# Performance work log

Measured on AMD Instinct MI355X. Metric: run time of the kernel, lower is better.

The kernel has to match this reference:

```python
import jax, jax.numpy as jnp
import numpy as np

WEIGHT = 1.0

# 3x3x3 discrete Laplacian stencil (6-connected, center -6), as in the torch module
_LAP_K = jnp.array(
    [[[0, 0, 0], [0, 1, 0], [0, 0, 0]],
     [[0, 1, 0], [1, -6, 1], [0, 1, 0]],
     [[0, 0, 0], [0, 1, 0], [0, 0, 0]]], dtype=jnp.float32)


def _abs_laplacian3d(x):
    """x: (N, D, H, W) -> |3D Laplacian(x)| with zero padding, same shape."""
    y = jax.lax.conv_general_dilated(
        x[:, None],              # (N, 1, D, H, W)
        _LAP_K[None, None],      # (1, 1, 3, 3, 3)
        window_strides=(1, 1, 1),
        padding=[(1, 1), (1, 1), (1, 1)])
    return jnp.abs(y[:, 0])


def setup_inputs() -> dict:
    key = jax.random.key(0)
    k1, k2 = jax.random.split(key)
    B, C, D, H, W = 2, 4, 64, 256, 256
    logits = jax.random.normal(k1, (B, C, D, H, W), dtype=jnp.float32)
    targets = jax.random.randint(k2, (B, D, H, W), 0, C)
    return {"logits": logits, "targets": targets}


def reference(logits, targets):
    B, C, D, H, W = logits.shape
    # softmax over class dim, drop background class 0 -> (B, C-1, D, H, W)
    probs = jax.nn.softmax(logits, axis=1)[:, 1:]
    # one-hot target masks for classes 1..C-1 -> (B, C-1, D, H, W)
    cls = jnp.arange(1, C)[None, :, None, None, None]
    tmask = (targets[:, None] == cls).astype(logits.dtype)
    # fused 3D Laplacian + abs over all (batch, class) pairs at once
    pred_b = _abs_laplacian3d(probs.reshape(B * (C - 1), D, H, W))
    targ_b = _abs_laplacian3d(tmask.reshape(B * (C - 1), D, H, W))
    # sum over classes of per-class MSE, divided by (C-1) == mean over everything
    return WEIGHT * jnp.mean((pred_b - targ_b) ** 2)
```

## Files before the change

### kernel.cpp

```cpp
#include <hip/hip_runtime.h>


#define CS   (1 << 22)
#define NTOT_INV (1.0f / 25165824.0f)
#define BIAS3 ((8 << 20) | (8 << 10) | 8)
#define BAR() asm volatile("s_waitcnt lgkmcnt(0)\n\ts_barrier" ::: "memory")

#define ISSUE(S, off)                                                        \
    S##0 = *(const float4*)(L + lBase + (off));                              \
    S##1 = *(const float4*)(L + lBase + (off) + CS);                         \
    S##2 = *(const float4*)(L + lBase + (off) + 2 * CS);                     \
    S##3 = *(const float4*)(L + lBase + (off) + 3 * CS);                     \
    S##t = *(const int4*)(T + tBase + (off));                                \
    if (hd) {                                                                \
        S##h0 = L[hlB + (off)];          S##h1 = L[hlB + (off) + CS];        \
        S##h2 = L[hlB + (off) + 2 * CS]; S##h3 = L[hlB + (off) + 3 * CS];    \
        S##hq = T[htB + (off)];                                              \
    }

__device__ __forceinline__ void smax1(float x0, float x1, float x2, float x3,
                                      float vm, float& p1, float& p2, float& p3) {
    float m  = fmaxf(fmaxf(x0, x1), fmaxf(x2, x3));
    float e0 = __expf(x0 - m);
    float e1 = __expf(x1 - m);
    float e2 = __expf(x2 - m);
    float e3 = __expf(x3 - m);
    float r  = vm * __builtin_amdgcn_rcpf(e0 + e1 + e2 + e3);
    p1 = e1 * r; p2 = e2 * r; p3 = e3 * r;
}

__device__ __forceinline__ int ohenc(int t, int msk) {
    int nz = (t > 0) ? 1 : 0;
    return (nz << (((t - 1) & 3) * 10)) & msk;
}

__global__ __launch_bounds__(256) void boundary_loss_kernel(
        const float* __restrict__ L,
        const int*   __restrict__ T,
        float*       __restrict__ out) {
    const int tid = threadIdx.x;
    const int tw  = tid & 7;
    const int th  = tid >> 3;

    const int bi    = blockIdx.x;
    const int wt    = bi & 7;
    const int dt    = (bi >> 3) & 15;
    const int colHi = bi >> 7;
    const int ht    = colHi % 9;
    const int b     = colHi / 9;

    const int   h0 = ht * 30;
    const int   h  = h0 + th - 1;
    const bool  hv = ((unsigned)h < 256u);
    const float vm = hv ? 1.f : 0.f;
    const int   ohm = hv ? ~0 : 0;
    const int   w0 = wt << 5;
    const int   sp = ((hv ? h : 0) << 8) | (w0 + (tw << 2));
    const int   tBase = b * CS + sp;
    const int   lBase = (b << 2) * CS + sp;
    const bool  live  = (th >= 1) && (th <= 30) && hv;
    const int   d0 = dt << 2;

    const bool  hd   = (tid < 60);
    const int   side = (tid >= 30) ? 1 : 0;
    const int   hr   = side ? (tid - 29) : (tid + 1);
    const int   hh   = h0 + hr - 1;
    const int   hwv  = side ? (w0 + 32) : (w0 - 1);
    const bool  hvv  = hd && ((unsigned)hh < 256u) && ((unsigned)hwv < 256u);
    const float hvm  = hvv ? 1.f : 0.f;
    const int   hohm = hvv ? ~0 : 0;
    const int   hsp  = ((hvv ? hh : 0) << 8) | (hvv ? hwv : 0);
    const int   htB  = b * CS + hsp;
    const int   hlB  = (b << 2) * CS + hsp;

    __shared__ float P1[32][32], P2[32][32], P3[32][32];
    __shared__ int   OHS[32][32];
    __shared__ float HL1[2][32], HL2[2][32], HL3[2][32];
    __shared__ int   HLO[2][32];

    const int c0 = tw << 2;
    const float* lp1 = (tw == 0) ? &HL1[0][th] : &P1[th][c0 - 1];
    const float* lp2 = (tw == 0) ? &HL2[0][th] : &P2[th][c0 - 1];
    const float* lp3 = (tw == 0) ? &HL3[0][th] : &P3[th][c0 - 1];
    const int*   lpo = (tw == 0) ? &HLO[0][th] : &OHS[th][c0 - 1];
    const float* rp1 = (tw == 7) ? &HL1[1][th] : &P1[th][c0 + 4];
    const float* rp2 = (tw == 7) ? &HL2[1][th] : &P2[th][c0 + 4];
    const float* rp3 = (tw == 7) ? &HL3[1][th] : &P3[th][c0 + 4];
    const int*   rpo = (tw == 7) ? &HLO[1][th] : &OHS[th][c0 + 4];

    float4 c1, c2, c3; int4 coh;
    float4 a1, a2, a3; int4 aoh;
    float hc1 = 0.f, hc2 = 0.f, hc3 = 0.f; int hco = 0;
    float accv = 0.f;

    {
        const int  off = (dt > 0 ? d0 - 1 : 0) << 16;
        const float svm  = (dt > 0) ? vm : 0.f;
        const int   sohm = (dt > 0) ? ohm : 0;
        float4 q0 = *(const float4*)(L + lBase + off);
        float4 q1 = *(const float4*)(L + lBase + off + CS);
        float4 q2 = *(const float4*)(L + lBase + off + 2 * CS);
        float4 q3 = *(const float4*)(L + lBase + off + 3 * CS);
        int4   qt = *(const int4*)(T + tBase + off);
        smax1(q0.x, q1.x, q2.x, q3.x, svm, a1.x, a2.x, a3.x);
        smax1(q0.y, q1.y, q2.y, q3.y, svm, a1.y, a2.y, a3.y);
        smax1(q0.z, q1.z, q2.z, q3.z, svm, a1.z, a2.z, a3.z);
        smax1(q0.w, q1.w, q2.w, q3.w, svm, a1.w, a2.w, a3.w);
        aoh.x = ohenc(qt.x, sohm) + BIAS3; aoh.y = ohenc(qt.y, sohm) + BIAS3;
        aoh.z = ohenc(qt.z, sohm) + BIAS3; aoh.w = ohenc(qt.w, sohm) + BIAS3;
    }

    {
        const int off = d0 << 16;
        float4 q0 = *(const float4*)(L + lBase + off);
        float4 q1 = *(const float4*)(L + lBase + off + CS);
        float4 q2 = *(const float4*)(L + lBase + off + 2 * CS);
        float4 q3 = *(const float4*)(L + lBase + off + 3 * CS);
        int4   qt = *(const int4*)(T + tBase + off);
        float hx0 = 0.f, hx1 = 0.f, hx2 = 0.f, hx3 = 0.f; int hqt = 0;
        if (hd) {
            hx0 = L[hlB + off]; hx1 = L[hlB + off + CS];
            hx2 = L[hlB + off + 2 * CS]; hx3 = L[hlB + off + 3 * CS];
            hqt = T[htB + off];
        }
        smax1(q0.x, q1.x, q2.x, q3.x, vm, c1.x, c2.x, c3.x);
        smax1(q0.y, q1.y, q2.y, q3.y, vm, c1.y, c2.y, c3.y);
        smax1(q0.z, q1.z, q2.z, q3.z, vm, c1.z, c2.z, c3.z);
        smax1(q0.w, q1.w, q2.w, q3.w, vm, c1.w, c2.w, c3.w);
        coh.x = ohenc(qt.x, ohm); coh.y = ohenc(qt.y, ohm);
        coh.z = ohenc(qt.z, ohm); coh.w = ohenc(qt.w, ohm);
        smax1(hx0, hx1, hx2, hx3, hvm, hc1, hc2, hc3);
        hco = ohenc(hqt, hohm);
    }

    float4 A0, A1, A2, A3; int4 At;
    float Ah0 = 0.f, Ah1 = 0.f, Ah2 = 0.f, Ah3 = 0.f; int Ahq = 0;
    {
        const int off = (d0 + 1 < 64 ? d0 + 1 : 63) << 16;
        ISSUE(A, off)
    }

#pragma unroll
    for (int i = 0; i < 4; ++i) {
        float4 B0, B1, B2, B3; int4 Bt;
        float Bh0 = 0.f, Bh1 = 0.f, Bh2 = 0.f, Bh3 = 0.f; int Bhq = 0;
        B0 = B1 = B2 = B3 = make_float4(0.f, 0.f, 0.f, 0.f);
        Bt = make_int4(0, 0, 0, 0);
        if (i < 3) {
            const int off = (d0 + i + 2 < 64 ? d0 + i + 2 : 63) << 16;
            ISSUE(B, off)
        }

        BAR();
        *(float4*)&P1[th][c0] = c1;
        *(float4*)&P2[th][c0] = c2;
        *(float4*)&P3[th][c0] = c3;
        *(int4*)&OHS[th][c0]  = coh;
        if (hd) {
            HL1[side][hr] = hc1; HL2[side][hr] = hc2; HL3[side][hr] = hc3;
            HLO[side][hr] = hco;
        }
        BAR();

        if (live) {
            float4 u, dn4; float lf, rt;
            u = *(float4*)&P1[th - 1][c0]; dn4 = *(float4*)&P1[th + 1][c0];
            lf = *lp1; rt = *rp1;
            a1.x += u.x + dn4.x + lf   + c1.y - 6.f * c1.x;
            a1.y += u.y + dn4.y + c1.x + c1.z - 6.f * c1.y;
            a1.z += u.z + dn4.z + c1.y + c1.w - 6.f * c1.z;
            a1.w += u.w + dn4.w + c1.z + rt   - 6.f * c1.w;
            u = *(float4*)&P2[th - 1][c0]; dn4 = *(float4*)&P2[th + 1][c0];
            lf = *lp2; rt = *rp2;
            a2.x += u.x + dn4.x + lf   + c2.y - 6.f * c2.x;
            a2.y += u.y + dn4.y + c2.x + c2.z - 6.f * c2.y;
            a2.z += u.z + dn4.z + c2.y + c2.w - 6.f * c2.z;
            a2.w += u.w + dn4.w + c2.z + rt   - 6.f * c2.w;
            u = *(float4*)&P3[th - 1][c0]; dn4 = *(float4*)&P3[th + 1][c0];
            lf = *lp3; rt = *rp3;
            a3.x += u.x + dn4.x + lf   + c3.y - 6.f * c3.x;
            a3.y += u.y + dn4.y + c3.x + c3.z - 6.f * c3.y;
            a3.z += u.z + dn4.z + c3.y + c3.w - 6.f * c3.z;
            a3.w += u.w + dn4.w + c3.z + rt   - 6.f * c3.w;

            int4 iu = *(int4*)&OHS[th - 1][c0];
            int4 id = *(int4*)&OHS[th + 1][c0];
            int  il = *lpo, ir = *rpo;
            aoh.x += iu.x + id.x + il    + coh.y - 6 * coh.x;
            aoh.y += iu.y + id.y + coh.x + coh.z - 6 * coh.y;
            aoh.z += iu.z + id.z + coh.y + coh.w - 6 * coh.z;
            aoh.w += iu.w + id.w + coh.z + ir    - 6 * coh.w;
        }

        const int   dnA   = d0 + i + 1;
        const float vmn   = (dnA < 64) ? vm : 0.f;
        const int   ohmn  = (dnA < 64) ? ohm : 0;
        const float hvmn  = (dnA < 64) ? hvm : 0.f;
        const int   hohmn = (dnA < 64) ? hohm : 0;
        float4 n1, n2, n3; int4 noh;
        smax1(A0.x, A1.x, A2.x, A3.x, vmn, n1.x, n2.x, n3.x);
        smax1(A0.y, A1.y, A2.y, A3.y, vmn, n1.y, n2.y, n3.y);
        smax1(A0.z, A1.z, A2.z, A3.z, vmn, n1.z, n2.z, n3.z);
        smax1(A0.w, A1.w, A2.w, A3.w, vmn, n1.w, n2.w, n3.w);
        noh.x = ohenc(At.x, ohmn); noh.y = ohenc(At.y, ohmn);
        noh.z = ohenc(At.z, ohmn); noh.w = ohenc(At.w, ohmn);
        float hn1, hn2, hn3;
        smax1(Ah0, Ah1, Ah2, Ah3, hvmn, hn1, hn2, hn3);
        int hno = ohenc(Ahq, hohmn);

        if (live) {
            int t0 = aoh.x + noh.x, t1 = aoh.y + noh.y;
            int t2 = aoh.z + noh.z, t3 = aoh.w + noh.w;
            float lp, lt, df;
            lp = fabsf(a1.x + n1.x); lt = fabsf((float)((t0 & 1023) - 8));          df = lp - lt; accv = fmaf(df, df, accv);
            lp = fabsf(a2.x + n2.x); lt = fabsf((float)(((t0 >> 10) & 1023) - 8));  df = lp - lt; accv = fmaf(df, df, accv);
            lp = fabsf(a3.x + n3.x); lt = fabsf((float)(((t0 >> 20) & 1023) - 8));  df = lp - lt; accv = fmaf(df, df, accv);
            lp = fabsf(a1.y + n1.y); lt = fabsf((float)((t1 & 1023) - 8));          df = lp - lt; accv = fmaf(df, df, accv);
            lp = fabsf(a2.y + n2.y); lt = fabsf((float)(((t1 >> 10) & 1023) - 8));  df = lp - lt; accv = fmaf(df, df, accv);
            lp = fabsf(a3.y + n3.y); lt = fabsf((float)(((t1 >> 20) & 1023) - 8));  df = lp - lt; accv = fmaf(df, df, accv);
            lp = fabsf(a1.z + n1.z); lt = fabsf((float)((t2 & 1023) - 8));          df = lp - lt; accv = fmaf(df, df, accv);
            lp = fabsf(a2.z + n2.z); lt = fabsf((float)(((t2 >> 10) & 1023) - 8));  df = lp - lt; accv = fmaf(df, df, accv);
            lp = fabsf(a3.z + n3.z); lt = fabsf((float)(((t2 >> 20) & 1023) - 8));  df = lp - lt; accv = fmaf(df, df, accv);
            lp = fabsf(a1.w + n1.w); lt = fabsf((float)((t3 & 1023) - 8));          df = lp - lt; accv = fmaf(df, df, accv);
            lp = fabsf(a2.w + n2.w); lt = fabsf((float)(((t3 >> 10) & 1023) - 8));  df = lp - lt; accv = fmaf(df, df, accv);
            lp = fabsf(a3.w + n3.w); lt = fabsf((float)(((t3 >> 20) & 1023) - 8));  df = lp - lt; accv = fmaf(df, df, accv);
        }

        a1 = c1; a2 = c2; a3 = c3;
        aoh.x = coh.x + BIAS3; aoh.y = coh.y + BIAS3;
        aoh.z = coh.z + BIAS3; aoh.w = coh.w + BIAS3;
        c1 = n1; c2 = n2; c3 = n3; coh = noh;
        hc1 = hn1; hc2 = hn2; hc3 = hn3; hco = hno;
        A0 = B0; A1 = B1; A2 = B2; A3 = B3; At = Bt;
        Ah0 = Bh0; Ah1 = Bh1; Ah2 = Bh2; Ah3 = Bh3; Ahq = Bhq;
    }

    for (int o = 32; o > 0; o >>= 1) accv += __shfl_down(accv, o, 64);
    __shared__ float wsum[4];
    if ((tid & 63) == 0) wsum[tid >> 6] = accv;
    __syncthreads();
    if (tid == 0)
        atomicAdd(out, (wsum[0] + wsum[1] + wsum[2] + wsum[3]) * NTOT_INV);
}

extern "C" void kernel_launch(void* const* d_in, const int* in_sizes, int n_in,
                              void* d_out, int out_size, void* d_ws, size_t ws_size,
                              hipStream_t stream) {
    const float* logits  = (const float*)d_in[0];
    const int*   targets = (const int*)d_in[1];
    float*       out     = (float*)d_out;

    hipMemsetAsync(out, 0, sizeof(float), stream);
    boundary_loss_kernel<<<2304, 256, 0, stream>>>(logits, targets, out);
}
```

Measured before the change: 235.6 us.

## Retile stencil to full-width rows with wavefront shuffles for W neighbors

Result: faster. 217.1 us (-7.9%).

```diff
diff --git a/kernel.cpp b/kernel.cpp
--- a/kernel.cpp
+++ b/kernel.cpp
@@ -11,12 +11,7 @@
     S##1 = *(const float4*)(L + lBase + (off) + CS);                         \
     S##2 = *(const float4*)(L + lBase + (off) + 2 * CS);                     \
     S##3 = *(const float4*)(L + lBase + (off) + 3 * CS);                     \
-    S##t = *(const int4*)(T + tBase + (off));                                \
-    if (hd) {                                                                \
-        S##h0 = L[hlB + (off)];          S##h1 = L[hlB + (off) + CS];        \
-        S##h2 = L[hlB + (off) + 2 * CS]; S##h3 = L[hlB + (off) + 3 * CS];    \
-        S##hq = T[htB + (off)];                                              \
-    }
+    S##t = *(const int4*)(T + tBase + (off));
 
 __device__ __forceinline__ void smax1(float x0, float x1, float x2, float x3,
                                       float vm, float& p1, float& p2, float& p3) {
@@ -34,74 +29,45 @@
     return (nz << (((t - 1) & 3) * 10)) & msk;
 }
 
-__global__ __launch_bounds__(256) void boundary_loss_kernel(
+__global__ __launch_bounds__(512) void boundary_loss_kernel(
         const float* __restrict__ L,
         const int*   __restrict__ T,
         float*       __restrict__ out) {
-    const int tid = threadIdx.x;
-    const int tw  = tid & 7;
-    const int th  = tid >> 3;
-
-    const int bi    = blockIdx.x;
-    const int wt    = bi & 7;
-    const int dt    = (bi >> 3) & 15;
-    const int colHi = bi >> 7;
-    const int ht    = colHi % 9;
-    const int b     = colHi / 9;
-
-    const int   h0 = ht * 30;
-    const int   h  = h0 + th - 1;
-    const bool  hv = ((unsigned)h < 256u);
-    const float vm = hv ? 1.f : 0.f;
+    const int tid  = threadIdx.x;
+    const int lane = tid & 63;
+    const int th   = tid >> 6;
+    int bi = blockIdx.x;
+    const int dseg = bi & 7;  bi >>= 3;
+    const int ht   = bi % 43;
+    const int b    = bi / 43;
+
+    const int   h   = ht * 6 + th - 1;
+    const bool  hv  = ((unsigned)h < 256u);
+    const int   hcl = min(max(h, 0), 255);
+    const float vm  = hv ? 1.f : 0.f;
     const int   ohm = hv ? ~0 : 0;
-    const int   w0 = wt << 5;
-    const int   sp = ((hv ? h : 0) << 8) | (w0 + (tw << 2));
-    const int   tBase = b * CS + sp;
-    const int   lBase = (b << 2) * CS + sp;
-    const bool  live  = (th >= 1) && (th <= 30) && hv;
-    const int   d0 = dt << 2;
-
-    const bool  hd   = (tid < 60);
-    const int   side = (tid >= 30) ? 1 : 0;
-    const int   hr   = side ? (tid - 29) : (tid + 1);
-    const int   hh   = h0 + hr - 1;
-    const int   hwv  = side ? (w0 + 32) : (w0 - 1);
-    const bool  hvv  = hd && ((unsigned)hh < 256u) && ((unsigned)hwv < 256u);
-    const float hvm  = hvv ? 1.f : 0.f;
-    const int   hohm = hvv ? ~0 : 0;
-    const int   hsp  = ((hvv ? hh : 0) << 8) | (hvv ? hwv : 0);
-    const int   htB  = b * CS + hsp;
-    const int   hlB  = (b << 2) * CS + hsp;
-
-    __shared__ float P1[32][32], P2[32][32], P3[32][32];
-    __shared__ int   OHS[32][32];
-    __shared__ float HL1[2][32], HL2[2][32], HL3[2][32];
-    __shared__ int   HLO[2][32];
-
-    const int c0 = tw << 2;
-    const float* lp1 = (tw == 0) ? &HL1[0][th] : &P1[th][c0 - 1];
-    const float* lp2 = (tw == 0) ? &HL2[0][th] : &P2[th][c0 - 1];
-    const float* lp3 = (tw == 0) ? &HL3[0][th] : &P3[th][c0 - 1];
-    const int*   lpo = (tw == 0) ? &HLO[0][th] : &OHS[th][c0 - 1];
-    const float* rp1 = (tw == 7) ? &HL1[1][th] : &P1[th][c0 + 4];
-    const float* rp2 = (tw == 7) ? &HL2[1][th] : &P2[th][c0 + 4];
-    const float* rp3 = (tw == 7) ? &HL3[1][th] : &P3[th][c0 + 4];
-    const int*   rpo = (tw == 7) ? &HLO[1][th] : &OHS[th][c0 + 4];
+    const bool  live = (th >= 1) && (th <= 6) && hv;
+    const int   d0  = dseg << 3;
+
+    const int rowoff = (hcl << 8) + (lane << 2);
+    const int tBase  = b * CS + rowoff;
+    const int lBase  = (b << 2) * CS + rowoff;
+
+    __shared__ float P1[8][256], P2[8][256], P3[8][256];
+    __shared__ int   OH[8][256];
+
+    const int c0 = lane << 2;
 
     float4 c1, c2, c3; int4 coh;
     float4 a1, a2, a3; int4 aoh;
-    float hc1 = 0.f, hc2 = 0.f, hc3 = 0.f; int hco = 0;
     float accv = 0.f;
 
     {
-        const int  off = (dt > 0 ? d0 - 1 : 0) << 16;
-        const float svm  = (dt > 0) ? vm : 0.f;
-        const int   sohm = (dt > 0) ? ohm : 0;
-        float4 q0 = *(const float4*)(L + lBase + off);
-        float4 q1 = *(const float4*)(L + lBase + off + CS);
-        float4 q2 = *(const float4*)(L + lBase + off + 2 * CS);
-        float4 q3 = *(const float4*)(L + lBase + off + 3 * CS);
-        int4   qt = *(const int4*)(T + tBase + off);
+        const int   off  = (dseg > 0 ? d0 - 1 : 0) << 16;
+        const float svm  = (dseg > 0) ? vm : 0.f;
+        const int   sohm = (dseg > 0) ? ohm : 0;
+        float4 q0, q1, q2, q3; int4 qt;
+        ISSUE(q, off)
         smax1(q0.x, q1.x, q2.x, q3.x, svm, a1.x, a2.x, a3.x);
         smax1(q0.y, q1.y, q2.y, q3.y, svm, a1.y, a2.y, a3.y);
         smax1(q0.z, q1.z, q2.z, q3.z, svm, a1.z, a2.z, a3.z);
@@ -112,41 +78,28 @@
 
     {
         const int off = d0 << 16;
-        float4 q0 = *(const float4*)(L + lBase + off);
-        float4 q1 = *(const float4*)(L + lBase + off + CS);
-        float4 q2 = *(const float4*)(L + lBase + off + 2 * CS);
-        float4 q3 = *(const float4*)(L + lBase + off + 3 * CS);
-        int4   qt = *(const int4*)(T + tBase + off);
-        float hx0 = 0.f, hx1 = 0.f, hx2 = 0.f, hx3 = 0.f; int hqt = 0;
-        if (hd) {
-            hx0 = L[hlB + off]; hx1 = L[hlB + off + CS];
-            hx2 = L[hlB + off + 2 * CS]; hx3 = L[hlB + off + 3 * CS];
-            hqt = T[htB + off];
-        }
+        float4 q0, q1, q2, q3; int4 qt;
+        ISSUE(q, off)
         smax1(q0.x, q1.x, q2.x, q3.x, vm, c1.x, c2.x, c3.x);
         smax1(q0.y, q1.y, q2.y, q3.y, vm, c1.y, c2.y, c3.y);
         smax1(q0.z, q1.z, q2.z, q3.z, vm, c1.z, c2.z, c3.z);
         smax1(q0.w, q1.w, q2.w, q3.w, vm, c1.w, c2.w, c3.w);
         coh.x = ohenc(qt.x, ohm); coh.y = ohenc(qt.y, ohm);
         coh.z = ohenc(qt.z, ohm); coh.w = ohenc(qt.w, ohm);
-        smax1(hx0, hx1, hx2, hx3, hvm, hc1, hc2, hc3);
-        hco = ohenc(hqt, hohm);
     }
 
     float4 A0, A1, A2, A3; int4 At;
-    float Ah0 = 0.f, Ah1 = 0.f, Ah2 = 0.f, Ah3 = 0.f; int Ahq = 0;
     {
         const int off = (d0 + 1 < 64 ? d0 + 1 : 63) << 16;
         ISSUE(A, off)
     }
 
 #pragma unroll
-    for (int i = 0; i < 4; ++i) {
+    for (int i = 0; i < 8; ++i) {
         float4 B0, B1, B2, B3; int4 Bt;
-        float Bh0 = 0.f, Bh1 = 0.f, Bh2 = 0.f, Bh3 = 0.f; int Bhq = 0;
         B0 = B1 = B2 = B3 = make_float4(0.f, 0.f, 0.f, 0.f);
         Bt = make_int4(0, 0, 0, 0);
-        if (i < 3) {
+        if (i < 7) {
             const int off = (d0 + i + 2 < 64 ? d0 + i + 2 : 63) << 16;
             ISSUE(B, off)
         }
@@ -155,48 +108,45 @@
         *(float4*)&P1[th][c0] = c1;
         *(float4*)&P2[th][c0] = c2;
         *(float4*)&P3[th][c0] = c3;
-        *(int4*)&OHS[th][c0]  = coh;
-        if (hd) {
-            HL1[side][hr] = hc1; HL2[side][hr] = hc2; HL3[side][hr] = hc3;
-            HLO[side][hr] = hco;
-        }
+        *(int4*)&OH[th][c0]   = coh;
         BAR();
 
         if (live) {
-            float4 u, dn4; float lf, rt;
-            u = *(float4*)&P1[th - 1][c0]; dn4 = *(float4*)&P1[th + 1][c0];
-            lf = *lp1; rt = *rp1;
-            a1.x += u.x + dn4.x + lf   + c1.y - 6.f * c1.x;
-            a1.y += u.y + dn4.y + c1.x + c1.z - 6.f * c1.y;
-            a1.z += u.z + dn4.z + c1.y + c1.w - 6.f * c1.z;
-            a1.w += u.w + dn4.w + c1.z + rt   - 6.f * c1.w;
-            u = *(float4*)&P2[th - 1][c0]; dn4 = *(float4*)&P2[th + 1][c0];
-            lf = *lp2; rt = *rp2;
-            a2.x += u.x + dn4.x + lf   + c2.y - 6.f * c2.x;
-            a2.y += u.y + dn4.y + c2.x + c2.z - 6.f * c2.y;
-            a2.z += u.z + dn4.z + c2.y + c2.w - 6.f * c2.z;
-            a2.w += u.w + dn4.w + c2.z + rt   - 6.f * c2.w;
-            u = *(float4*)&P3[th - 1][c0]; dn4 = *(float4*)&P3[th + 1][c0];
-            lf = *lp3; rt = *rp3;
-            a3.x += u.x + dn4.x + lf   + c3.y - 6.f * c3.x;
-            a3.y += u.y + dn4.y + c3.x + c3.z - 6.f * c3.y;
-            a3.z += u.z + dn4.z + c3.y + c3.w - 6.f * c3.z;
-            a3.w += u.w + dn4.w + c3.z + rt   - 6.f * c3.w;
-
-            int4 iu = *(int4*)&OHS[th - 1][c0];
-            int4 id = *(int4*)&OHS[th + 1][c0];
-            int  il = *lpo, ir = *rpo;
-            aoh.x += iu.x + id.x + il    + coh.y - 6 * coh.x;
+            float l1 = __shfl_up(c1.w, 1, 64);   float r1 = __shfl_down(c1.x, 1, 64);
+            float l2 = __shfl_up(c2.w, 1, 64);   float r2 = __shfl_down(c2.x, 1, 64);
+            float l3 = __shfl_up(c3.w, 1, 64);   float r3 = __shfl_down(c3.x, 1, 64);
+            int   lo = __shfl_up(coh.w, 1, 64);  int   ro = __shfl_down(coh.x, 1, 64);
+            if (lane == 0)  { l1 = l2 = l3 = 0.f; lo = 0; }
+            if (lane == 63) { r1 = r2 = r3 = 0.f; ro = 0; }
+
+            float4 u, v;
+            u = *(float4*)&P1[th - 1][c0]; v = *(float4*)&P1[th + 1][c0];
+            a1.x += u.x + v.x + l1   + c1.y - 6.f * c1.x;
+            a1.y += u.y + v.y + c1.x + c1.z - 6.f * c1.y;
+            a1.z += u.z + v.z + c1.y + c1.w - 6.f * c1.z;
+            a1.w += u.w + v.w + c1.z + r1   - 6.f * c1.w;
+            u = *(float4*)&P2[th - 1][c0]; v = *(float4*)&P2[th + 1][c0];
+            a2.x += u.x + v.x + l2   + c2.y - 6.f * c2.x;
+            a2.y += u.y + v.y + c2.x + c2.z - 6.f * c2.y;
+            a2.z += u.z + v.z + c2.y + c2.w - 6.f * c2.z;
+            a2.w += u.w + v.w + c2.z + r2   - 6.f * c2.w;
+            u = *(float4*)&P3[th - 1][c0]; v = *(float4*)&P3[th + 1][c0];
+            a3.x += u.x + v.x + l3   + c3.y - 6.f * c3.x;
+            a3.y += u.y + v.y + c3.x + c3.z - 6.f * c3.y;
+            a3.z += u.z + v.z + c3.y + c3.w - 6.f * c3.z;
+            a3.w += u.w + v.w + c3.z + r3   - 6.f * c3.w;
+
+            int4 iu = *(int4*)&OH[th - 1][c0];
+            int4 id = *(int4*)&OH[th + 1][c0];
+            aoh.x += iu.x + id.x + lo    + coh.y - 6 * coh.x;
             aoh.y += iu.y + id.y + coh.x + coh.z - 6 * coh.y;
             aoh.z += iu.z + id.z + coh.y + coh.w - 6 * coh.z;
-            aoh.w += iu.w + id.w + coh.z + ir    - 6 * coh.w;
+            aoh.w += iu.w + id.w + coh.z + ro    - 6 * coh.w;
         }
 
-        const int   dnA   = d0 + i + 1;
-        const float vmn   = (dnA < 64) ? vm : 0.f;
-        const int   ohmn  = (dnA < 64) ? ohm : 0;
-        const float hvmn  = (dnA < 64) ? hvm : 0.f;
-        const int   hohmn = (dnA < 64) ? hohm : 0;
+        const int   dnA  = d0 + i + 1;
+        const float vmn  = (dnA < 64) ? vm : 0.f;
+        const int   ohmn = (dnA < 64) ? ohm : 0;
         float4 n1, n2, n3; int4 noh;
         smax1(A0.x, A1.x, A2.x, A3.x, vmn, n1.x, n2.x, n3.x);
         smax1(A0.y, A1.y, A2.y, A3.y, vmn, n1.y, n2.y, n3.y);
@@ -204,9 +154,6 @@
         smax1(A0.w, A1.w, A2.w, A3.w, vmn, n1.w, n2.w, n3.w);
         noh.x = ohenc(At.x, ohmn); noh.y = ohenc(At.y, ohmn);
         noh.z = ohenc(At.z, ohmn); noh.w = ohenc(At.w, ohmn);
-        float hn1, hn2, hn3;
-        smax1(Ah0, Ah1, Ah2, Ah3, hvmn, hn1, hn2, hn3);
-        int hno = ohenc(Ahq, hohmn);
 
         if (live) {
             int t0 = aoh.x + noh.x, t1 = aoh.y + noh.y;
@@ -230,17 +177,18 @@
         aoh.x = coh.x + BIAS3; aoh.y = coh.y + BIAS3;
         aoh.z = coh.z + BIAS3; aoh.w = coh.w + BIAS3;
         c1 = n1; c2 = n2; c3 = n3; coh = noh;
-        hc1 = hn1; hc2 = hn2; hc3 = hn3; hco = hno;
         A0 = B0; A1 = B1; A2 = B2; A3 = B3; At = Bt;
-        Ah0 = Bh0; Ah1 = Bh1; Ah2 = Bh2; Ah3 = Bh3; Ahq = Bhq;
     }
 
     for (int o = 32; o > 0; o >>= 1) accv += __shfl_down(accv, o, 64);
-    __shared__ float wsum[4];
-    if ((tid & 63) == 0) wsum[tid >> 6] = accv;
+    __shared__ float wsum[8];
+    if (lane == 0) wsum[th] = accv;
     __syncthreads();
-    if (tid == 0)
-        atomicAdd(out, (wsum[0] + wsum[1] + wsum[2] + wsum[3]) * NTOT_INV);
+    if (tid == 0) {
+        float s = wsum[0] + wsum[1] + wsum[2] + wsum[3]
+                + wsum[4] + wsum[5] + wsum[6] + wsum[7];
+        atomicAdd(out, s * NTOT_INV);
+    }
 }
 
 extern "C" void kernel_launch(void* const* d_in, const int* in_sizes, int n_in,
@@ -251,5 +199,5 @@
     float*       out     = (float*)d_out;
 
     hipMemsetAsync(out, 0, sizeof(float), stream);
-    boundary_loss_kernel<<<2304, 256, 0, stream>>>(logits, targets, out);
-}
+    boundary_loss_kernel<<<688, 512, 0, stream>>>(logits, targets, out);
+}
```
